# Kernel optimization log

Measured on AMD Instinct MI355X. Metric: run time of the kernel, lower is better.

Reference implementation:

```python
import jax, jax.numpy as jnp
import numpy as np

NUM_LAYERS = 10
HIDDEN = 5
INPUT = 5
SEQ = 457
OUT = 457


def _lstm_layer(x_tbi, W_ih, W_hh, b):
    # x_tbi: [T, B, in]; W_ih: [4H, in]; W_hh: [4H, H]; b: [4H] (b_ih + b_hh)
    B = x_tbi.shape[1]
    h0 = jnp.zeros((B, HIDDEN), x_tbi.dtype)
    c0 = jnp.zeros((B, HIDDEN), x_tbi.dtype)
    # precompute input projections for all timesteps: [T, B, 4H]
    xW = jnp.einsum('tbi,gi->tbg', x_tbi, W_ih) + b

    def step(carry, xw_t):
        h, c = carry
        gates = xw_t + h @ W_hh.T  # [B, 4H]
        i, f, g, o = jnp.split(gates, 4, axis=-1)  # PyTorch gate order i,f,g,o
        i = jax.nn.sigmoid(i)
        f = jax.nn.sigmoid(f)
        g = jnp.tanh(g)
        o = jax.nn.sigmoid(o)
        c = f * c + i * g
        h = o * jnp.tanh(c)
        return (h, c), h

    (_, _), hs = jax.lax.scan(step, (h0, c0), xW)
    return hs  # [T, B, H]


def setup_inputs() -> dict:
    key = jax.random.key(0)
    ks = jax.random.split(key, 8)
    B = 4096
    x = jax.random.normal(ks[0], (B, SEQ, INPUT), dtype=jnp.float32)
    attn = jnp.ones((B, SEQ), dtype=jnp.int64)
    tok = jnp.zeros((B, SEQ), dtype=jnp.int64)
    s = 1.0 / np.sqrt(HIDDEN)
    # layer 0 input size == HIDDEN, so all layers stack uniformly
    W_ih = jax.random.uniform(ks[1], (NUM_LAYERS, 4 * HIDDEN, INPUT), jnp.float32, -s, s)
    W_hh = jax.random.uniform(ks[2], (NUM_LAYERS, 4 * HIDDEN, HIDDEN), jnp.float32, -s, s)
    b_ih = jax.random.uniform(ks[3], (NUM_LAYERS, 4 * HIDDEN), jnp.float32, -s, s)
    b_hh = jax.random.uniform(ks[4], (NUM_LAYERS, 4 * HIDDEN), jnp.float32, -s, s)
    sf = 1.0 / np.sqrt(HIDDEN * SEQ)
    fc_W = jax.random.uniform(ks[5], (OUT, HIDDEN * SEQ), jnp.float32, -sf, sf)
    fc_b = jax.random.uniform(ks[6], (OUT,), jnp.float32, -sf, sf)
    return {"a_input_ids": x, "a_attention_mask": attn, "a_token_type_ids": tok,
            "W_ih": W_ih, "W_hh": W_hh, "b_ih": b_ih, "b_hh": b_hh,
            "fc_W": fc_W, "fc_b": fc_b}


def reference(a_input_ids, a_attention_mask, a_token_type_ids, W_ih, W_hh, b_ih, b_hh, fc_W, fc_b):
    x = jnp.transpose(a_input_ids.astype(jnp.float32), (1, 0, 2))  # [T, B, 5]
    b = b_ih + b_hh
    for l in range(NUM_LAYERS):
        x = _lstm_layer(x, W_ih[l], W_hh[l], b[l])  # [T, B, H]
    out = jnp.transpose(x, (1, 0, 2))  # [B, T, H]
    flat = out.reshape(out.shape[0], -1)  # [B, T*H]
    # dropout is identity at inference
    return flat @ fc_W.T + fc_b  # [B, OUT]
```

## Files before the change

kernel.cpp:

```cpp
#include <hip/hip_runtime.h>

#define NUM_LAYERS 10
#define HIDDEN 5
#define SEQ 457
#define BATCH 4096
#define OUT_DIM 457
#define KD 2285
#define KPAD 2304
#define NKT 72
#define OPAD 512

typedef __attribute__((ext_vector_type(8))) short short8;
typedef __attribute__((ext_vector_type(4))) float f32x4;

__device__ __forceinline__ float frcp(float x){ return __builtin_amdgcn_rcpf(x); }
__device__ __forceinline__ float sigm(float x){ return frcp(1.0f + __expf(-x)); }
__device__ __forceinline__ float tanh_(float x){ return 1.0f - 2.0f*frcp(1.0f + __expf(2.0f*x)); }
__device__ __forceinline__ unsigned short f2bf(float f){
    unsigned u = __float_as_uint(f);
    u = (u + 0x7FFFu + ((u>>16)&1u)) >> 16;
    return (unsigned short)u;
}
__device__ __forceinline__ float bf2f(unsigned short h){
    return __uint_as_float(((unsigned)h) << 16);
}

#define WAVES_PER_BLOCK 4
__global__ __launch_bounds__(64*WAVES_PER_BLOCK) void lstm_kernel(
    const float* __restrict__ x,
    const float* __restrict__ W_ih,
    const float* __restrict__ W_hh,
    const float* __restrict__ b_ih,
    const float* __restrict__ b_hh,
    unsigned short* __restrict__ Hb)
{
    const int lane = threadIdx.x & 63;
    const int wv = threadIdx.x >> 6;
    const int b = blockIdx.x * WAVES_PER_BLOCK + wv;
    const int l = lane / 5;
    const int j = lane - 5 * l;
    const bool isCell = lane < 50;
    const bool isGhost = (lane >= 50) && (lane < 55);
    const int lc = isCell ? l : 0;

    unsigned short* Hrow = Hb + (size_t)b * KPAD;
    if (lane < KPAD - KD) Hrow[KD + lane] = 0;

    float wih[4][5], whh[4][5], bb[4];
#pragma unroll
    for (int q = 0; q < 4; ++q) {
        const int row = lc * 20 + q * HIDDEN + j;
#pragma unroll
        for (int i = 0; i < 5; ++i) {
            wih[q][i] = W_ih[row * 5 + i];
            whh[q][i] = W_hh[row * 5 + i];
        }
        bb[q] = b_ih[row] + b_hh[row];
    }

    const int baseH = 5 * l;
    const int baseI = (l == 0) ? 50 : (baseH - 5);
    int iH[5], iI[5];
#pragma unroll
    for (int i = 0; i < 5; ++i) { iH[i] = (baseH + i) * 4; iI[i] = (baseI + i) * 4; }

    const float* xb = x + (size_t)b * (SEQ * HIDDEN);

    float hmsg = 0.0f, c = 0.0f;
    float xv = 0.0f;
    if (isGhost) {
        hmsg = xb[lane - 50];
        xv   = xb[5 + (lane - 50)];
    }

    for (int s = 0; s < SEQ + NUM_LAYERS - 1; ++s) {
        const int hbits = __float_as_int(hmsg);
        float in[5], hp[5];
#pragma unroll
        for (int i = 0; i < 5; ++i)
            in[i] = __int_as_float(__builtin_amdgcn_ds_bpermute(iI[i], hbits));
#pragma unroll
        for (int i = 0; i < 5; ++i)
            hp[i] = __int_as_float(__builtin_amdgcn_ds_bpermute(iH[i], hbits));

        const int t = s - l;

        float g0 = bb[0], g1 = bb[1], g2 = bb[2], g3 = bb[3];
#pragma unroll
        for (int i = 0; i < 5; ++i) {
            g0 = fmaf(wih[0][i], in[i], g0);
            g1 = fmaf(wih[1][i], in[i], g1);
            g2 = fmaf(wih[2][i], in[i], g2);
            g3 = fmaf(wih[3][i], in[i], g3);
        }
#pragma unroll
        for (int i = 0; i < 5; ++i) {
            g0 = fmaf(whh[0][i], hp[i], g0);
            g1 = fmaf(whh[1][i], hp[i], g1);
            g2 = fmaf(whh[2][i], hp[i], g2);
            g3 = fmaf(whh[3][i], hp[i], g3);
        }
        const float ig = sigm(g0);
        const float fg = sigm(g1);
        const float gg = tanh_(g2);
        const float og = sigm(g3);

        if (isCell && t >= 0 && t < SEQ) {
            c = fg * c + ig * gg;
            const float h = og * tanh_(c);
            hmsg = h;
            if (l == NUM_LAYERS - 1) Hrow[t * 5 + j] = f2bf(h);
        }
        if (isGhost) {
            hmsg = xv;
            int t2 = s + 2; if (t2 > SEQ - 1) t2 = SEQ - 1;
            xv = xb[t2 * 5 + (lane - 50)];
        }
    }
}

__global__ __launch_bounds__(256) void convw_kernel(
    const float* __restrict__ fcW,
    unsigned short* __restrict__ Whi,
    unsigned short* __restrict__ Wlo)
{
    const int idx = blockIdx.x * 256 + threadIdx.x;
    if (idx >= OPAD * KPAD) return;
    const int o = idx / KPAD;
    const int k = idx - o * KPAD;
    float v = 0.0f;
    if (o < OUT_DIM && k < KD) v = fcW[o * KD + k];
    const unsigned short hi = f2bf(v);
    const float rem = v - bf2f(hi);
    Whi[idx] = hi;
    Wlo[idx] = f2bf(rem);
}

__global__ __launch_bounds__(256) void fc_kernel(
    const unsigned short* __restrict__ Hb,
    const unsigned short* __restrict__ Whi,
    const unsigned short* __restrict__ Wlo,
    const float* __restrict__ fcb,
    float* __restrict__ out)
{
    const int lane = threadIdx.x & 63;
    const int w = threadIdx.x >> 6;
    const int b0 = blockIdx.x * 64 + w * 16;
    const int o0 = blockIdx.y * 64;
    const int row = lane & 15;
    const int kq = (lane >> 4) * 8;

    const unsigned short* Ha = Hb + (size_t)(b0 + row) * KPAD + kq;
    const unsigned short* Wh0 = Whi + (size_t)(o0 + row) * KPAD + kq;
    const unsigned short* Wl0 = Wlo + (size_t)(o0 + row) * KPAD + kq;

    f32x4 acc0 = {0.f, 0.f, 0.f, 0.f};
    f32x4 acc1 = {0.f, 0.f, 0.f, 0.f};
    f32x4 acc2 = {0.f, 0.f, 0.f, 0.f};
    f32x4 acc3 = {0.f, 0.f, 0.f, 0.f};

    for (int kk = 0; kk < NKT; ++kk) {
        const int kb = kk * 32;
        const short8 a = *(const short8*)(Ha + kb);

        const short8 wh0 = *(const short8*)(Wh0 + kb);
        const short8 wh1 = *(const short8*)(Wh0 + 16 * KPAD + kb);
        const short8 wh2 = *(const short8*)(Wh0 + 32 * KPAD + kb);
        const short8 wh3 = *(const short8*)(Wh0 + 48 * KPAD + kb);
        const short8 wl0 = *(const short8*)(Wl0 + kb);
        const short8 wl1 = *(const short8*)(Wl0 + 16 * KPAD + kb);
        const short8 wl2 = *(const short8*)(Wl0 + 32 * KPAD + kb);
        const short8 wl3 = *(const short8*)(Wl0 + 48 * KPAD + kb);

        acc0 = __builtin_amdgcn_mfma_f32_16x16x32_bf16(a, wh0, acc0, 0, 0, 0);
        acc1 = __builtin_amdgcn_mfma_f32_16x16x32_bf16(a, wh1, acc1, 0, 0, 0);
        acc2 = __builtin_amdgcn_mfma_f32_16x16x32_bf16(a, wh2, acc2, 0, 0, 0);
        acc3 = __builtin_amdgcn_mfma_f32_16x16x32_bf16(a, wh3, acc3, 0, 0, 0);
        acc0 = __builtin_amdgcn_mfma_f32_16x16x32_bf16(a, wl0, acc0, 0, 0, 0);
        acc1 = __builtin_amdgcn_mfma_f32_16x16x32_bf16(a, wl1, acc1, 0, 0, 0);
        acc2 = __builtin_amdgcn_mfma_f32_16x16x32_bf16(a, wl2, acc2, 0, 0, 0);
        acc3 = __builtin_amdgcn_mfma_f32_16x16x32_bf16(a, wl3, acc3, 0, 0, 0);
    }

    const int ocol = lane & 15;
    const int br0 = (lane >> 4) * 4;
#pragma unroll
    for (int nb = 0; nb < 4; ++nb) {
        const int o = o0 + nb * 16 + ocol;
        if (o < OUT_DIM) {
            const float bias = fcb[o];
            const f32x4 acc = (nb == 0) ? acc0 : (nb == 1) ? acc1 : (nb == 2) ? acc2 : acc3;
#pragma unroll
            for (int r = 0; r < 4; ++r) {
                const int bi = b0 + br0 + r;
                out[(size_t)bi * OUT_DIM + o] = acc[r] + bias;
            }
        }
    }
}

extern "C" void kernel_launch(void* const* d_in, const int* in_sizes, int n_in,
                              void* d_out, int out_size, void* d_ws, size_t ws_size,
                              hipStream_t stream) {
    const float* x    = (const float*)d_in[0];
    const float* W_ih = (const float*)d_in[3];
    const float* W_hh = (const float*)d_in[4];
    const float* b_ih = (const float*)d_in[5];
    const float* b_hh = (const float*)d_in[6];
    const float* fcW  = (const float*)d_in[7];
    const float* fcb  = (const float*)d_in[8];
    float* out = (float*)d_out;

    unsigned short* Hb  = (unsigned short*)d_ws;
    unsigned short* Whi = (unsigned short*)((char*)d_ws + (size_t)BATCH * KPAD * 2);
    unsigned short* Wlo = (unsigned short*)((char*)d_ws + (size_t)BATCH * KPAD * 2 + (size_t)OPAD * KPAD * 2);

    lstm_kernel<<<dim3(BATCH / WAVES_PER_BLOCK), dim3(64 * WAVES_PER_BLOCK), 0, stream>>>(
        x, W_ih, W_hh, b_ih, b_hh, Hb);

    convw_kernel<<<dim3((OPAD * KPAD + 255) / 256), dim3(256), 0, stream>>>(fcW, Whi, Wlo);

    fc_kernel<<<dim3(BATCH / 64, OPAD / 64), dim3(256), 0, stream>>>(Hb, Whi, Wlo, fcb, out);
}
```

Baseline: 594.0 us.

## Compute LSTM gates with MFMA over 16-sample batch groups via LDS wavefront pipeline

```diff
diff --git a/kernel.cpp b/kernel.cpp
--- a/kernel.cpp
+++ b/kernel.cpp
@@ -14,8 +14,7 @@
 typedef __attribute__((ext_vector_type(4))) float f32x4;
 
 __device__ __forceinline__ float frcp(float x){ return __builtin_amdgcn_rcpf(x); }
-__device__ __forceinline__ float sigm(float x){ return frcp(1.0f + __expf(-x)); }
-__device__ __forceinline__ float tanh_(float x){ return 1.0f - 2.0f*frcp(1.0f + __expf(2.0f*x)); }
+__device__ __forceinline__ float fexp2(float x){ return __builtin_amdgcn_exp2f(x); }
 __device__ __forceinline__ unsigned short f2bf(float f){
     unsigned u = __float_as_uint(f);
     u = (u + 0x7FFFu + ((u>>16)&1u)) >> 16;
@@ -25,8 +24,13 @@
     return __uint_as_float(((unsigned)h) << 16);
 }
 
-#define WAVES_PER_BLOCK 4
-__global__ __launch_bounds__(64*WAVES_PER_BLOCK) void lstm_kernel(
+#define GB 16
+#define NW 11
+#define CSTRIDE 20
+#define SLOTB (GB*CSTRIDE)
+#define BUFS (NUM_LAYERS*SLOTB)
+
+__global__ __launch_bounds__(64*NW) void lstm_kernel(
     const float* __restrict__ x,
     const float* __restrict__ W_ih,
     const float* __restrict__ W_hh,
@@ -34,88 +38,163 @@
     const float* __restrict__ b_hh,
     unsigned short* __restrict__ Hb)
 {
-    const int lane = threadIdx.x & 63;
-    const int wv = threadIdx.x >> 6;
-    const int b = blockIdx.x * WAVES_PER_BLOCK + wv;
-    const int l = lane / 5;
-    const int j = lane - 5 * l;
-    const bool isCell = lane < 50;
-    const bool isGhost = (lane >= 50) && (lane < 55);
-    const int lc = isCell ? l : 0;
-
-    unsigned short* Hrow = Hb + (size_t)b * KPAD;
-    if (lane < KPAD - KD) Hrow[KD + lane] = 0;
-
-    float wih[4][5], whh[4][5], bb[4];
-#pragma unroll
-    for (int q = 0; q < 4; ++q) {
-        const int row = lc * 20 + q * HIDDEN + j;
-#pragma unroll
-        for (int i = 0; i < 5; ++i) {
-            wih[q][i] = W_ih[row * 5 + i];
-            whh[q][i] = W_hh[row * 5 + i];
-        }
-        bb[q] = b_ih[row] + b_hh[row];
+    __shared__ unsigned short Cs[2*BUFS];
+    const int tid = threadIdx.x;
+    const int wv = tid >> 6;
+    const int lane = tid & 63;
+    const int bBlk = blockIdx.x * GB;
+
+    for (int i = tid; i < 2*BUFS; i += 64*NW) Cs[i] = 0;
+    __syncthreads();
+
+    const int m  = lane & 15;
+    const int kg = lane >> 4;
+    short8 wf0, wf1;
+    f32x4 bias0, bias1;
+    int off0 = 0, off1 = 0;
+    float c0 = 0.f, c1 = 0.f;
+    float xr[5];
+    const float* xb = nullptr;
+
+    if (wv < NUM_LAYERS) {
+        const int l = wv;
+        {
+            const int j = m >> 2, g = m & 3;
+            const float scg = (g == 2) ? 2.8853900817779268f : -1.4426950408889634f;
+            const int row = l*20 + g*5 + j;
+#pragma unroll
+            for (int e = 0; e < 8; ++e) {
+                const int k = kg*8 + e;
+                unsigned short v = 0;
+                if (k < 30) {
+                    const int ki = (k < 10) ? k : (k < 20) ? k-10 : k-20;
+                    const float w = scg * ((ki < 5) ? W_ih[row*5+ki] : W_hh[row*5+ki-5]);
+                    const unsigned short hi = f2bf(w);
+                    v = (k >= 20) ? f2bf(w - bf2f(hi)) : hi;
+                }
+                wf0[e] = (short)v;
+            }
+        }
+        {
+#pragma unroll
+            for (int e = 0; e < 8; ++e) {
+                unsigned short v = 0;
+                if (m < 4) {
+                    const int g = m;
+                    const float scg = (g == 2) ? 2.8853900817779268f : -1.4426950408889634f;
+                    const int row = l*20 + g*5 + 4;
+                    const int k = kg*8 + e;
+                    if (k < 30) {
+                        const int ki = (k < 10) ? k : (k < 20) ? k-10 : k-20;
+                        const float w = scg * ((ki < 5) ? W_ih[row*5+ki] : W_hh[row*5+ki-5]);
+                        const unsigned short hi = f2bf(w);
+                        v = (k >= 20) ? f2bf(w - bf2f(hi)) : hi;
+                    }
+                }
+                wf1[e] = (short)v;
+            }
+        }
+#pragma unroll
+        for (int r = 0; r < 4; ++r) {
+            const float scg = (r == 2) ? 2.8853900817779268f : -1.4426950408889634f;
+            bias0[r] = scg * (b_ih[wv*20 + r*5 + kg] + b_hh[wv*20 + r*5 + kg]);
+            bias1[r] = (kg == 0) ? scg * (b_ih[wv*20 + r*5 + 4] + b_hh[wv*20 + r*5 + 4]) : 0.f;
+        }
+        off0 = (kg==0) ? 0 : (kg==1) ? 16 : (kg==2) ? 32 : 8;
+        off1 = (kg==0) ? 8 : (kg==1) ? 24 : (kg==2) ? 0 : 16;
+    } else {
+        const int b = lane & 15;
+        xb = x + (size_t)(bBlk + b) * (SEQ*HIDDEN);
+        for (int i = lane; i < GB*(KPAD-KD); i += 64) {
+            const int bb = i / (KPAD-KD), cc = i - bb*(KPAD-KD);
+            Hb[(size_t)(bBlk+bb)*KPAD + KD + cc] = 0;
+        }
+        if (lane < GB) {
+            unsigned short* cw = &Cs[0*BUFS + 0*SLOTB + b*CSTRIDE];
+#pragma unroll
+            for (int i = 0; i < 5; ++i) {
+                const float xv = xb[i];
+                const unsigned short hi = f2bf(xv);
+                cw[i] = hi;
+                cw[10+i] = f2bf(xv - bf2f(hi));
+            }
+#pragma unroll
+            for (int i = 0; i < 5; ++i) xr[i] = xb[5 + i];
+        }
     }
-
-    const int baseH = 5 * l;
-    const int baseI = (l == 0) ? 50 : (baseH - 5);
-    int iH[5], iI[5];
-#pragma unroll
-    for (int i = 0; i < 5; ++i) { iH[i] = (baseH + i) * 4; iI[i] = (baseI + i) * 4; }
-
-    const float* xb = x + (size_t)b * (SEQ * HIDDEN);
-
-    float hmsg = 0.0f, c = 0.0f;
-    float xv = 0.0f;
-    if (isGhost) {
-        hmsg = xb[lane - 50];
-        xv   = xb[5 + (lane - 50)];
-    }
+    __syncthreads();
 
     for (int s = 0; s < SEQ + NUM_LAYERS - 1; ++s) {
-        const int hbits = __float_as_int(hmsg);
-        float in[5], hp[5];
-#pragma unroll
-        for (int i = 0; i < 5; ++i)
-            in[i] = __int_as_float(__builtin_amdgcn_ds_bpermute(iI[i], hbits));
-#pragma unroll
-        for (int i = 0; i < 5; ++i)
-            hp[i] = __int_as_float(__builtin_amdgcn_ds_bpermute(iH[i], hbits));
-
-        const int t = s - l;
-
-        float g0 = bb[0], g1 = bb[1], g2 = bb[2], g3 = bb[3];
-#pragma unroll
-        for (int i = 0; i < 5; ++i) {
-            g0 = fmaf(wih[0][i], in[i], g0);
-            g1 = fmaf(wih[1][i], in[i], g1);
-            g2 = fmaf(wih[2][i], in[i], g2);
-            g3 = fmaf(wih[3][i], in[i], g3);
-        }
-#pragma unroll
-        for (int i = 0; i < 5; ++i) {
-            g0 = fmaf(whh[0][i], hp[i], g0);
-            g1 = fmaf(whh[1][i], hp[i], g1);
-            g2 = fmaf(whh[2][i], hp[i], g2);
-            g3 = fmaf(whh[3][i], hp[i], g3);
-        }
-        const float ig = sigm(g0);
-        const float fg = sigm(g1);
-        const float gg = tanh_(g2);
-        const float og = sigm(g3);
-
-        if (isCell && t >= 0 && t < SEQ) {
-            c = fg * c + ig * gg;
-            const float h = og * tanh_(c);
-            hmsg = h;
-            if (l == NUM_LAYERS - 1) Hrow[t * 5 + j] = f2bf(h);
-        }
-        if (isGhost) {
-            hmsg = xv;
-            int t2 = s + 2; if (t2 > SEQ - 1) t2 = SEQ - 1;
-            xv = xb[t2 * 5 + (lane - 50)];
-        }
+        if (wv < NUM_LAYERS) {
+            const int l = wv;
+            const char* cb = (const char*)&Cs[(s&1)*BUFS + l*SLOTB + m*CSTRIDE];
+            union { short8 s8; unsigned long u[2]; } bv;
+            bv.u[0] = *(const unsigned long*)(cb + off0);
+            bv.u[1] = *(const unsigned long*)(cb + off1);
+
+            f32x4 d0 = __builtin_amdgcn_mfma_f32_16x16x32_bf16(wf0, bv.s8, bias0, 0, 0, 0);
+            f32x4 d2 = __builtin_amdgcn_mfma_f32_16x16x32_bf16(wf1, bv.s8, bias1, 0, 0, 0);
+
+            const float ig  = frcp(1.f + fexp2(d0[0]));
+            const float fg  = frcp(1.f + fexp2(d0[1]));
+            const float gg  = 1.f - 2.f*frcp(1.f + fexp2(d0[2]));
+            const float og  = frcp(1.f + fexp2(d0[3]));
+            const float ig1 = frcp(1.f + fexp2(d2[0]));
+            const float fg1 = frcp(1.f + fexp2(d2[1]));
+            const float gg1 = 1.f - 2.f*frcp(1.f + fexp2(d2[2]));
+            const float og1 = frcp(1.f + fexp2(d2[3]));
+
+            const int t = s - l;
+            if (t >= 0 && t < SEQ) {
+                c0 = fg*c0 + ig*gg;
+                const float th0 = 1.f - 2.f*frcp(1.f + fexp2(2.8853900817779268f*c0));
+                const float h0 = og*th0;
+                c1 = fg1*c1 + ig1*gg1;
+                const float th1 = 1.f - 2.f*frcp(1.f + fexp2(2.8853900817779268f*c1));
+                const float h1 = og1*th1;
+
+                const unsigned short h0hi = f2bf(h0);
+                const unsigned short h0lo = f2bf(h0 - bf2f(h0hi));
+                const unsigned short h1hi = f2bf(h1);
+                const unsigned short h1lo = f2bf(h1 - bf2f(h1hi));
+
+                unsigned short* wb = &Cs[((s+1)&1)*BUFS];
+                unsigned short* myslot = wb + l*SLOTB + m*CSTRIDE;
+                const int j = kg;
+                myslot[5+j]  = h0hi;
+                myslot[15+j] = h0lo;
+                if (l < NUM_LAYERS-1) {
+                    unsigned short* nx = wb + (l+1)*SLOTB + m*CSTRIDE;
+                    nx[j]    = h0hi;
+                    nx[10+j] = h0lo;
+                    if (kg == 0) { nx[4] = h1hi; nx[14] = h1lo; }
+                }
+                if (kg == 0) { myslot[5+4] = h1hi; myslot[15+4] = h1lo; }
+                if (l == NUM_LAYERS-1) {
+                    unsigned short* hr = Hb + (size_t)(bBlk + m)*KPAD + t*5;
+                    hr[j] = h0hi;
+                    if (kg == 0) hr[4] = h1hi;
+                }
+            }
+        } else {
+            const int b = lane & 15;
+            if (lane < GB) {
+                const int tw = s + 1;
+                if (tw < SEQ) {
+                    unsigned short* cw = &Cs[((s+1)&1)*BUFS + 0*SLOTB + b*CSTRIDE];
+#pragma unroll
+                    for (int i = 0; i < 5; ++i) {
+                        const unsigned short hi = f2bf(xr[i]);
+                        cw[i] = hi;
+                        cw[10+i] = f2bf(xr[i] - bf2f(hi));
+                    }
+                }
+                int t2 = s + 2; if (t2 > SEQ-1) t2 = SEQ-1;
+#pragma unroll
+                for (int i = 0; i < 5; ++i) xr[i] = xb[t2*5 + i];
+            }
+        }
+        __syncthreads();
     }
 }
 
@@ -131,9 +210,8 @@
     float v = 0.0f;
     if (o < OUT_DIM && k < KD) v = fcW[o * KD + k];
     const unsigned short hi = f2bf(v);
-    const float rem = v - bf2f(hi);
     Whi[idx] = hi;
-    Wlo[idx] = f2bf(rem);
+    Wlo[idx] = f2bf(v - bf2f(hi));
 }
 
 __global__ __launch_bounds__(256) void fc_kernel(
@@ -150,36 +228,46 @@
     const int row = lane & 15;
     const int kq = (lane >> 4) * 8;
 
-    const unsigned short* Ha = Hb + (size_t)(b0 + row) * KPAD + kq;
+    const unsigned short* Ha  = Hb  + (size_t)(b0 + row) * KPAD + kq;
     const unsigned short* Wh0 = Whi + (size_t)(o0 + row) * KPAD + kq;
     const unsigned short* Wl0 = Wlo + (size_t)(o0 + row) * KPAD + kq;
 
-    f32x4 acc0 = {0.f, 0.f, 0.f, 0.f};
-    f32x4 acc1 = {0.f, 0.f, 0.f, 0.f};
-    f32x4 acc2 = {0.f, 0.f, 0.f, 0.f};
-    f32x4 acc3 = {0.f, 0.f, 0.f, 0.f};
+    f32x4 acc0 = {0.f,0.f,0.f,0.f}, acc1 = acc0, acc2 = acc0, acc3 = acc0;
+
+    short8 a_c   = *(const short8*)(Ha);
+    short8 wh0_c = *(const short8*)(Wh0);
+    short8 wh1_c = *(const short8*)(Wh0 + 16*KPAD);
+    short8 wh2_c = *(const short8*)(Wh0 + 32*KPAD);
+    short8 wh3_c = *(const short8*)(Wh0 + 48*KPAD);
+    short8 wl0_c = *(const short8*)(Wl0);
+    short8 wl1_c = *(const short8*)(Wl0 + 16*KPAD);
+    short8 wl2_c = *(const short8*)(Wl0 + 32*KPAD);
+    short8 wl3_c = *(const short8*)(Wl0 + 48*KPAD);
 
     for (int kk = 0; kk < NKT; ++kk) {
-        const int kb = kk * 32;
-        const short8 a = *(const short8*)(Ha + kb);
-
-        const short8 wh0 = *(const short8*)(Wh0 + kb);
-        const short8 wh1 = *(const short8*)(Wh0 + 16 * KPAD + kb);
-        const short8 wh2 = *(const short8*)(Wh0 + 32 * KPAD + kb);
-        const short8 wh3 = *(const short8*)(Wh0 + 48 * KPAD + kb);
-        const short8 wl0 = *(const short8*)(Wl0 + kb);
-        const short8 wl1 = *(const short8*)(Wl0 + 16 * KPAD + kb);
-        const short8 wl2 = *(const short8*)(Wl0 + 32 * KPAD + kb);
-        const short8 wl3 = *(const short8*)(Wl0 + 48 * KPAD + kb);
-
-        acc0 = __builtin_amdgcn_mfma_f32_16x16x32_bf16(a, wh0, acc0, 0, 0, 0);
-        acc1 = __builtin_amdgcn_mfma_f32_16x16x32_bf16(a, wh1, acc1, 0, 0, 0);
-        acc2 = __builtin_amdgcn_mfma_f32_16x16x32_bf16(a, wh2, acc2, 0, 0, 0);
-        acc3 = __builtin_amdgcn_mfma_f32_16x16x32_bf16(a, wh3, acc3, 0, 0, 0);
-        acc0 = __builtin_amdgcn_mfma_f32_16x16x32_bf16(a, wl0, acc0, 0, 0, 0);
-        acc1 = __builtin_amdgcn_mfma_f32_16x16x32_bf16(a, wl1, acc1, 0, 0, 0);
-        acc2 = __builtin_amdgcn_mfma_f32_16x16x32_bf16(a, wl2, acc2, 0, 0, 0);
-        acc3 = __builtin_amdgcn_mfma_f32_16x16x32_bf16(a, wl3, acc3, 0, 0, 0);
+        const int kb = (kk+1 < NKT) ? (kk+1)*32 : kk*32;
+        const short8 a_n   = *(const short8*)(Ha  + kb);
+        const short8 wh0_n = *(const short8*)(Wh0 + kb);
+        const short8 wh1_n = *(const short8*)(Wh0 + 16*KPAD + kb);
+        const short8 wh2_n = *(const short8*)(Wh0 + 32*KPAD + kb);
+        const short8 wh3_n = *(const short8*)(Wh0 + 48*KPAD + kb);
+        const short8 wl0_n = *(const short8*)(Wl0 + kb);
+        const short8 wl1_n = *(const short8*)(Wl0 + 16*KPAD + kb);
+        const short8 wl2_n = *(const short8*)(Wl0 + 32*KPAD + kb);
+        const short8 wl3_n = *(const short8*)(Wl0 + 48*KPAD + kb);
+
+        acc0 = __builtin_amdgcn_mfma_f32_16x16x32_bf16(a_c, wh0_c, acc0, 0,0,0);
+        acc1 = __builtin_amdgcn_mfma_f32_16x16x32_bf16(a_c, wh1_c, acc1, 0,0,0);
+        acc2 = __builtin_amdgcn_mfma_f32_16x16x32_bf16(a_c, wh2_c, acc2, 0,0,0);
+        acc3 = __builtin_amdgcn_mfma_f32_16x16x32_bf16(a_c, wh3_c, acc3, 0,0,0);
+        acc0 = __builtin_amdgcn_mfma_f32_16x16x32_bf16(a_c, wl0_c, acc0, 0,0,0);
+        acc1 = __builtin_amdgcn_mfma_f32_16x16x32_bf16(a_c, wl1_c, acc1, 0,0,0);
+        acc2 = __builtin_amdgcn_mfma_f32_16x16x32_bf16(a_c, wl2_c, acc2, 0,0,0);
+        acc3 = __builtin_amdgcn_mfma_f32_16x16x32_bf16(a_c, wl3_c, acc3, 0,0,0);
+
+        a_c = a_n;
+        wh0_c = wh0_n; wh1_c = wh1_n; wh2_c = wh2_n; wh3_c = wh3_n;
+        wl0_c = wl0_n; wl1_c = wl1_n; wl2_c = wl2_n; wl3_c = wl3_n;
     }
 
     const int ocol = lane & 15;
@@ -215,7 +303,7 @@
     unsigned short* Whi = (unsigned short*)((char*)d_ws + (size_t)BATCH * KPAD * 2);
     unsigned short* Wlo = (unsigned short*)((char*)d_ws + (size_t)BATCH * KPAD * 2 + (size_t)OPAD * KPAD * 2);
 
-    lstm_kernel<<<dim3(BATCH / WAVES_PER_BLOCK), dim3(64 * WAVES_PER_BLOCK), 0, stream>>>(
+    lstm_kernel<<<dim3(BATCH / GB), dim3(64 * NW), 0, stream>>>(
         x, W_ih, W_hh, b_ih, b_hh, Hb);
 
     convw_kernel<<<dim3((OPAD * KPAD + 255) / 256), dim3(256), 0, stream>>>(fcW, Whi, Wlo);
```

Result: faster. 553.4 us (-6.8%).
